# Performance work log

Measured on AMD Instinct MI355X. Metric: run time of the kernel, lower is better.

The kernel has to match this reference:

```python
import jax, jax.numpy as jnp
import numpy as np

NTOKENS = 50257
NHID = 1024
TPC = int(np.ceil(np.sqrt(NTOKENS)))          # 225 tokens per class
NCLASSES = int(np.ceil(NTOKENS / TPC))        # 224 classes
BATCH = 2048
INITRANGE = 0.1


def setup_inputs() -> dict:
    key = jax.random.key(0)
    k1, k2, k3, k4 = jax.random.split(key, 4)
    inputs = jax.random.normal(k1, (BATCH, NHID), dtype=jnp.float32)
    labels = jax.random.randint(k2, (BATCH,), 0, NTOKENS, dtype=jnp.int32)
    W_top = jax.random.uniform(k3, (NHID, NCLASSES), dtype=jnp.float32,
                               minval=-INITRANGE, maxval=INITRANGE)
    b_top = jnp.zeros((NCLASSES,), dtype=jnp.float32)
    W_bottom = jax.random.uniform(k4, (NCLASSES, NHID, TPC), dtype=jnp.float32,
                                  minval=-INITRANGE, maxval=INITRANGE)
    b_bottom = jnp.zeros((NCLASSES, TPC), dtype=jnp.float32)
    return {"inputs": inputs, "labels": labels, "W_top": W_top, "b_top": b_top,
            "W_bottom": W_bottom, "b_bottom": b_bottom}


def reference(inputs, labels, W_top, b_top, W_bottom, b_bottom):
    # Two-level hierarchical softmax: P(word) = P(class | h) * P(word | class, h)
    batch = inputs.shape[0]
    cls = labels // TPC          # [B] class index at top level
    word = labels % TPC          # [B] word index within class

    # Top level: [B, nclasses]
    top_probs = jax.nn.softmax(inputs @ W_top + b_top, axis=1)
    p_cls = top_probs[jnp.arange(batch), cls]            # [B]

    # Bottom level: gather per-example class weights then batched matvec
    Wb = W_bottom[cls]                                    # [B, nhid, tpc]
    bb = b_bottom[cls]                                    # [B, tpc]
    bottom_logits = jnp.einsum('bd,bdk->bk', inputs, Wb) + bb
    bottom_probs = jax.nn.softmax(bottom_logits, axis=1)
    p_word = bottom_probs[jnp.arange(batch), word]        # [B]

    return p_cls * p_word
```

## Files before the change

kernel.cpp:

```cpp
#include <hip/hip_runtime.h>
#include <math.h>

#define TPC 225
#define NCLS 224
#define NHID 1024
#define BATCH 2048
#define CAP 256

__global__ __launch_bounds__(256) void hs_bucket(const int* __restrict__ labels,
                                                 int* __restrict__ bucket,
                                                 int* __restrict__ cnt) {
    __shared__ int scnt[NCLS];
    const int t = threadIdx.x;
    for (int i = t; i < NCLS; i += 256) scnt[i] = 0;
    __syncthreads();
    for (int b = t; b < BATCH; b += 256) {
        int lab = labels[b];
        int c = lab / TPC;
        int w = lab - c * TPC;
        int pos = atomicAdd(&scnt[c], 1);
        bucket[c * CAP + pos] = (w << 16) | b;
    }
    __syncthreads();
    for (int i = t; i < NCLS; i += 256) cnt[i] = scnt[i];
}

template <int R, int WS, int NS>
__device__ __forceinline__ void gemm_softmax_rows(const float* const xrow[R],
                                                  const float* __restrict__ W,
                                                  const float* __restrict__ bias,
                                                  const int lane,
                                                  float prob[R][4]) {
    int kc[4];
#pragma unroll
    for (int j = 0; j < 4; j++) {
        int k = lane + 64 * j;
        kc[j] = (k < NS) ? k : (NS - 1);
    }
    float bs[4];
#pragma unroll
    for (int j = 0; j < 4; j++) bs[j] = bias[kc[j]];

    const float* wj[4];
#pragma unroll
    for (int j = 0; j < 4; j++) wj[j] = W + kc[j];
    const float* xr[R];
#pragma unroll
    for (int r = 0; r < R; r++) xr[r] = xrow[r];

    float wb[4][4][4];
    float4 xb[4][R];
    float acc[R][4];
#pragma unroll
    for (int r = 0; r < R; r++)
#pragma unroll
        for (int j = 0; j < 4; j++) acc[r][j] = 0.f;

#pragma unroll
    for (int b = 0; b < 4; b++) {
#pragma unroll
        for (int dd = 0; dd < 4; dd++)
#pragma unroll
            for (int j = 0; j < 4; j++) wb[b][dd][j] = wj[j][dd * WS];
#pragma unroll
        for (int r = 0; r < R; r++) xb[b][r] = *(const float4*)(xr[r]);
#pragma unroll
        for (int j = 0; j < 4; j++) wj[j] += 4 * WS;
#pragma unroll
        for (int r = 0; r < R; r++) xr[r] += 4;
    }

    for (int it = 0; it < 63; it++) {
#pragma unroll
        for (int b = 0; b < 4; b++) {
#pragma unroll
            for (int dd = 0; dd < 4; dd++)
#pragma unroll
                for (int r = 0; r < R; r++) {
                    float xv = ((const float*)&xb[b][r])[dd];
#pragma unroll
                    for (int j = 0; j < 4; j++)
                        acc[r][j] = fmaf(xv, wb[b][dd][j], acc[r][j]);
                }
#pragma unroll
            for (int dd = 0; dd < 4; dd++)
#pragma unroll
                for (int j = 0; j < 4; j++) wb[b][dd][j] = wj[j][dd * WS];
#pragma unroll
            for (int r = 0; r < R; r++) xb[b][r] = *(const float4*)(xr[r]);
#pragma unroll
            for (int j = 0; j < 4; j++) wj[j] += 4 * WS;
#pragma unroll
            for (int r = 0; r < R; r++) xr[r] += 4;
        }
    }

#pragma unroll
    for (int b = 0; b < 4; b++) {
#pragma unroll
        for (int dd = 0; dd < 4; dd++)
#pragma unroll
            for (int r = 0; r < R; r++) {
                float xv = ((const float*)&xb[b][r])[dd];
#pragma unroll
                for (int j = 0; j < 4; j++)
                    acc[r][j] = fmaf(xv, wb[b][dd][j], acc[r][j]);
            }
    }

#pragma unroll
    for (int r = 0; r < R; r++) {
        float lg[4];
#pragma unroll
        for (int j = 0; j < 4; j++) {
            int k = lane + 64 * j;
            lg[j] = (k < NS) ? acc[r][j] + bs[j] : -INFINITY;
        }
        float m = fmaxf(fmaxf(lg[0], lg[1]), fmaxf(lg[2], lg[3]));
#pragma unroll
        for (int off = 32; off > 0; off >>= 1) m = fmaxf(m, __shfl_xor(m, off, 64));
        float s = 0.f;
        float e[4];
#pragma unroll
        for (int j = 0; j < 4; j++) {
            int k = lane + 64 * j;
            e[j] = (k < NS) ? __expf(lg[j] - m) : 0.f;
            s += e[j];
        }
#pragma unroll
        for (int off = 32; off > 0; off >>= 1) s += __shfl_xor(s, off, 64);
        float inv = 1.f / s;
#pragma unroll
        for (int j = 0; j < 4; j++) prob[r][j] = e[j] * inv;
    }
}

__global__ __launch_bounds__(256, 1) void hs_top(const float* __restrict__ x,
                                                 const int* __restrict__ labels,
                                                 const float* __restrict__ W,
                                                 const float* __restrict__ bias,
                                                 float* __restrict__ pcls) {
    const int t = threadIdx.x;
    const int lane = t & 63;
    const int wave = t >> 6;
    const int r0 = blockIdx.x * 8 + wave * 2;

    const float* xrow[2] = {x + (size_t)r0 * NHID, x + (size_t)(r0 + 1) * NHID};
    float prob[2][4];
    gemm_softmax_rows<2, NCLS, NCLS>(xrow, W, bias, lane, prob);

#pragma unroll
    for (int r = 0; r < 2; r++) {
        int row = r0 + r;
        int c = labels[row] / TPC;
#pragma unroll
        for (int j = 0; j < 4; j++)
            if (lane + 64 * j == c) pcls[row] = prob[r][j];
    }
}

template <int R>
__device__ __forceinline__ void bottom_tile(const float* __restrict__ x,
                                            const float* __restrict__ Wc,
                                            const float* __restrict__ bbc,
                                            const int* __restrict__ bucket_c,
                                            const int n, const int base,
                                            const int lane, const int wave,
                                            const float* __restrict__ pcls,
                                            float* __restrict__ out) {
    const int i0 = base + wave * R;
    const float* xrow[R];
    int rowid[R], word[R];
#pragma unroll
    for (int r = 0; r < R; r++) {
        int idx = i0 + r;
        int packed = (idx < n) ? bucket_c[idx] : 0;
        rowid[r] = packed & 0xffff;
        word[r] = packed >> 16;
        xrow[r] = x + (size_t)rowid[r] * NHID;
    }
    float prob[R][4];
    gemm_softmax_rows<R, TPC, TPC>(xrow, Wc, bbc, lane, prob);
#pragma unroll
    for (int r = 0; r < R; r++) {
        if (i0 + r < n) {
#pragma unroll
            for (int j = 0; j < 4; j++)
                if (lane + 64 * j == word[r])
                    out[rowid[r]] = pcls[rowid[r]] * prob[r][j];
        }
    }
}

__global__ __launch_bounds__(256, 1) void hs_bottom(const float* __restrict__ x,
                                                    const float* __restrict__ Wb,
                                                    const float* __restrict__ bb,
                                                    const int* __restrict__ bucket,
                                                    const int* __restrict__ cnt,
                                                    const float* __restrict__ pcls,
                                                    float* __restrict__ out) {
    const int c = blockIdx.x;
    const int n = cnt[c];
    if (n == 0) return;
    const int t = threadIdx.x;
    const int lane = t & 63;
    const int wave = t >> 6;
    const float* Wc = Wb + (size_t)c * (NHID * TPC);
    const float* bbc = bb + c * TPC;
    const int* bucket_c = bucket + c * CAP;

    int R = (n + 3) >> 2;
    if (R > 8) R = 8;
    const int chunk = 4 * R;
    for (int base = 0; base < n; base += chunk) {
        switch (R) {
            case 1: bottom_tile<1>(x, Wc, bbc, bucket_c, n, base, lane, wave, pcls, out); break;
            case 2: bottom_tile<2>(x, Wc, bbc, bucket_c, n, base, lane, wave, pcls, out); break;
            case 3: bottom_tile<3>(x, Wc, bbc, bucket_c, n, base, lane, wave, pcls, out); break;
            case 4: bottom_tile<4>(x, Wc, bbc, bucket_c, n, base, lane, wave, pcls, out); break;
            case 5: bottom_tile<5>(x, Wc, bbc, bucket_c, n, base, lane, wave, pcls, out); break;
            case 6: bottom_tile<6>(x, Wc, bbc, bucket_c, n, base, lane, wave, pcls, out); break;
            case 7: bottom_tile<7>(x, Wc, bbc, bucket_c, n, base, lane, wave, pcls, out); break;
            default: bottom_tile<8>(x, Wc, bbc, bucket_c, n, base, lane, wave, pcls, out); break;
        }
    }
}

extern "C" void kernel_launch(void* const* d_in, const int* in_sizes, int n_in,
                              void* d_out, int out_size, void* d_ws, size_t ws_size,
                              hipStream_t stream) {
    const float* inputs   = (const float*)d_in[0];
    const int*   labels   = (const int*)d_in[1];
    const float* W_top    = (const float*)d_in[2];
    const float* b_top    = (const float*)d_in[3];
    const float* W_bottom = (const float*)d_in[4];
    const float* b_bottom = (const float*)d_in[5];
    float* out = (float*)d_out;

    int* bucket = (int*)d_ws;
    int* cnt    = bucket + NCLS * CAP;
    float* pcls = (float*)(cnt + NCLS);

    hs_bucket<<<1, 256, 0, stream>>>(labels, bucket, cnt);
    hs_top<<<BATCH / 8, 256, 0, stream>>>(inputs, labels, W_top, b_top, pcls);
    hs_bottom<<<NCLS, 256, 0, stream>>>(inputs, W_bottom, b_bottom, bucket, cnt,
                                        pcls, out);
}
```

Measured before the change: 467.4 us.

## Split logits GEMMs across column tiles and defer softmax to a finish kernel

Top and bottom logit computation now split output columns into four tiles per block, so each lane computes one column over several rows and the grid grows fourfold (NCLS*4 bottom blocks instead of NCLS). Raw logits go to a workspace buffer, and a new finish kernel applies bias, both softmaxes and the final product. Bottom-level rows are spread across waves in strips of up to four, with launch bounds raised to allow two blocks per CU. This aims to fix the poor parallelism of one block per class. The cost is an extra kernel launch, a workspace round trip of the logits, and re-reading x once per column tile.

Result: slower. 509.5 us (+9.0%).

```diff
diff --git a/kernel.cpp b/kernel.cpp
--- a/kernel.cpp
+++ b/kernel.cpp
@@ -6,6 +6,7 @@
 #define NHID 1024
 #define BATCH 2048
 #define CAP 256
+#define LSTRIDE 256
 
 __global__ __launch_bounds__(256) void hs_bucket(const int* __restrict__ labels,
                                                  int* __restrict__ bucket,
@@ -17,213 +18,202 @@
     for (int b = t; b < BATCH; b += 256) {
         int lab = labels[b];
         int c = lab / TPC;
-        int w = lab - c * TPC;
         int pos = atomicAdd(&scnt[c], 1);
-        bucket[c * CAP + pos] = (w << 16) | b;
+        bucket[c * CAP + pos] = b;
     }
     __syncthreads();
     for (int i = t; i < NCLS; i += 256) cnt[i] = scnt[i];
 }
 
-template <int R, int WS, int NS>
-__device__ __forceinline__ void gemm_softmax_rows(const float* const xrow[R],
-                                                  const float* __restrict__ W,
-                                                  const float* __restrict__ bias,
-                                                  const int lane,
-                                                  float prob[R][4]) {
-    int kc[4];
-#pragma unroll
-    for (int j = 0; j < 4; j++) {
-        int k = lane + 64 * j;
-        kc[j] = (k < NS) ? k : (NS - 1);
-    }
-    float bs[4];
-#pragma unroll
-    for (int j = 0; j < 4; j++) bs[j] = bias[kc[j]];
-
-    const float* wj[4];
-#pragma unroll
-    for (int j = 0; j < 4; j++) wj[j] = W + kc[j];
-    const float* xr[R];
-#pragma unroll
-    for (int r = 0; r < R; r++) xr[r] = xrow[r];
-
-    float wb[4][4][4];
-    float4 xb[4][R];
-    float acc[R][4];
-#pragma unroll
-    for (int r = 0; r < R; r++)
-#pragma unroll
-        for (int j = 0; j < 4; j++) acc[r][j] = 0.f;
-
-#pragma unroll
-    for (int b = 0; b < 4; b++) {
-#pragma unroll
-        for (int dd = 0; dd < 4; dd++)
-#pragma unroll
-            for (int j = 0; j < 4; j++) wb[b][dd][j] = wj[j][dd * WS];
-#pragma unroll
-        for (int r = 0; r < R; r++) xb[b][r] = *(const float4*)(xr[r]);
-#pragma unroll
-        for (int j = 0; j < 4; j++) wj[j] += 4 * WS;
-#pragma unroll
-        for (int r = 0; r < R; r++) xr[r] += 4;
-    }
-
-    for (int it = 0; it < 63; it++) {
-#pragma unroll
-        for (int b = 0; b < 4; b++) {
-#pragma unroll
-            for (int dd = 0; dd < 4; dd++)
-#pragma unroll
-                for (int r = 0; r < R; r++) {
-                    float xv = ((const float*)&xb[b][r])[dd];
-#pragma unroll
-                    for (int j = 0; j < 4; j++)
-                        acc[r][j] = fmaf(xv, wb[b][dd][j], acc[r][j]);
-                }
-#pragma unroll
-            for (int dd = 0; dd < 4; dd++)
-#pragma unroll
-                for (int j = 0; j < 4; j++) wb[b][dd][j] = wj[j][dd * WS];
-#pragma unroll
-            for (int r = 0; r < R; r++) xb[b][r] = *(const float4*)(xr[r]);
-#pragma unroll
-            for (int j = 0; j < 4; j++) wj[j] += 4 * WS;
-#pragma unroll
-            for (int r = 0; r < R; r++) xr[r] += 4;
-        }
-    }
-
-#pragma unroll
-    for (int b = 0; b < 4; b++) {
-#pragma unroll
-        for (int dd = 0; dd < 4; dd++)
+template <int R, int WS>
+__device__ __forceinline__ void kloop(const float* __restrict__ wp,
+                                      const float* const xp[R],
+                                      float acc[R]) {
+    constexpr int NG = NHID / 8;
+    float wv[4][8];
+    float4 xv[2][R][2];
+#pragma unroll
+    for (int r = 0; r < R; r++) acc[r] = 0.f;
+
+#pragma unroll
+    for (int b = 0; b < 4; b++)
+#pragma unroll
+        for (int u = 0; u < 8; u++) wv[b][u] = wp[(size_t)(b * 8 + u) * WS];
+#pragma unroll
+    for (int b = 0; b < 2; b++)
+#pragma unroll
+        for (int r = 0; r < R; r++) {
+            xv[b][r][0] = *(const float4*)(xp[r] + b * 8);
+            xv[b][r][1] = *(const float4*)(xp[r] + b * 8 + 4);
+        }
+    const float* wiss = wp + (size_t)32 * WS;
+    const float* xiss[R];
+#pragma unroll
+    for (int r = 0; r < R; r++) xiss[r] = xp[r] + 16;
+
+#pragma unroll 4
+    for (int g = 0; g < NG - 4; ++g) {
+        const int b = g & 3, xb = g & 1;
+#pragma unroll
+        for (int u = 0; u < 8; u++) {
+            const float w_u = wv[b][u];
 #pragma unroll
             for (int r = 0; r < R; r++) {
-                float xv = ((const float*)&xb[b][r])[dd];
-#pragma unroll
-                for (int j = 0; j < 4; j++)
-                    acc[r][j] = fmaf(xv, wb[b][dd][j], acc[r][j]);
+                const float xval = ((const float*)&xv[xb][r][u >> 2])[u & 3];
+                acc[r] = fmaf(xval, w_u, acc[r]);
             }
-    }
-
-#pragma unroll
-    for (int r = 0; r < R; r++) {
-        float lg[4];
-#pragma unroll
-        for (int j = 0; j < 4; j++) {
-            int k = lane + 64 * j;
-            lg[j] = (k < NS) ? acc[r][j] + bs[j] : -INFINITY;
-        }
-        float m = fmaxf(fmaxf(lg[0], lg[1]), fmaxf(lg[2], lg[3]));
-#pragma unroll
-        for (int off = 32; off > 0; off >>= 1) m = fmaxf(m, __shfl_xor(m, off, 64));
-        float s = 0.f;
-        float e[4];
-#pragma unroll
-        for (int j = 0; j < 4; j++) {
-            int k = lane + 64 * j;
-            e[j] = (k < NS) ? __expf(lg[j] - m) : 0.f;
-            s += e[j];
-        }
-#pragma unroll
-        for (int off = 32; off > 0; off >>= 1) s += __shfl_xor(s, off, 64);
-        float inv = 1.f / s;
-#pragma unroll
-        for (int j = 0; j < 4; j++) prob[r][j] = e[j] * inv;
-    }
-}
-
-__global__ __launch_bounds__(256, 1) void hs_top(const float* __restrict__ x,
-                                                 const int* __restrict__ labels,
-                                                 const float* __restrict__ W,
-                                                 const float* __restrict__ bias,
-                                                 float* __restrict__ pcls) {
+        }
+#pragma unroll
+        for (int u = 0; u < 8; u++) wv[b][u] = wiss[(size_t)u * WS];
+        wiss += 8 * WS;
+#pragma unroll
+        for (int r = 0; r < R; r++) {
+            xv[xb][r][0] = *(const float4*)(xiss[r]);
+            xv[xb][r][1] = *(const float4*)(xiss[r] + 4);
+            xiss[r] += 8;
+        }
+    }
+#pragma unroll
+    for (int g = NG - 4; g < NG; ++g) {
+        const int b = g & 3, xb = g & 1;
+#pragma unroll
+        for (int u = 0; u < 8; u++) {
+            const float w_u = wv[b][u];
+#pragma unroll
+            for (int r = 0; r < R; r++) {
+                const float xval = ((const float*)&xv[xb][r][u >> 2])[u & 3];
+                acc[r] = fmaf(xval, w_u, acc[r]);
+            }
+        }
+        if (g + 2 < NG) {
+#pragma unroll
+            for (int r = 0; r < R; r++) {
+                xv[xb][r][0] = *(const float4*)(xiss[r]);
+                xv[xb][r][1] = *(const float4*)(xiss[r] + 4);
+                xiss[r] += 8;
+            }
+        }
+    }
+}
+
+__global__ __launch_bounds__(256, 2) void hs_tlogits(const float* __restrict__ x,
+                                                     const float* __restrict__ W,
+                                                     float* __restrict__ tws) {
     const int t = threadIdx.x;
     const int lane = t & 63;
     const int wave = t >> 6;
-    const int r0 = blockIdx.x * 8 + wave * 2;
-
-    const float* xrow[2] = {x + (size_t)r0 * NHID, x + (size_t)(r0 + 1) * NHID};
-    float prob[2][4];
-    gemm_softmax_rows<2, NCLS, NCLS>(xrow, W, bias, lane, prob);
-
-#pragma unroll
-    for (int r = 0; r < 2; r++) {
-        int row = r0 + r;
-        int c = labels[row] / TPC;
-#pragma unroll
-        for (int j = 0; j < 4; j++)
-            if (lane + 64 * j == c) pcls[row] = prob[r][j];
+    const int r0 = (blockIdx.x >> 2) * 16 + wave * 4;
+    const int tile = blockIdx.x & 3;
+    const int col = tile * 56 + lane;
+    const int colc = (lane < 56) ? col : (NCLS - 1);
+
+    const float* xp[4];
+#pragma unroll
+    for (int r = 0; r < 4; r++) xp[r] = x + (size_t)(r0 + r) * NHID;
+    float acc[4];
+    kloop<4, NCLS>(W + colc, xp, acc);
+    if (lane < 56) {
+#pragma unroll
+        for (int r = 0; r < 4; r++) tws[(size_t)(r0 + r) * LSTRIDE + col] = acc[r];
     }
 }
 
 template <int R>
-__device__ __forceinline__ void bottom_tile(const float* __restrict__ x,
-                                            const float* __restrict__ Wc,
-                                            const float* __restrict__ bbc,
-                                            const int* __restrict__ bucket_c,
-                                            const int n, const int base,
-                                            const int lane, const int wave,
-                                            const float* __restrict__ pcls,
-                                            float* __restrict__ out) {
-    const int i0 = base + wave * R;
-    const float* xrow[R];
-    int rowid[R], word[R];
+__device__ __forceinline__ void btile(const float* __restrict__ x,
+                                      const float* __restrict__ Wcol,
+                                      const int* __restrict__ bucket_c,
+                                      const int base, const int col,
+                                      float* __restrict__ bws) {
+    int rowid[R];
+    const float* xp[R];
 #pragma unroll
     for (int r = 0; r < R; r++) {
-        int idx = i0 + r;
-        int packed = (idx < n) ? bucket_c[idx] : 0;
-        rowid[r] = packed & 0xffff;
-        word[r] = packed >> 16;
-        xrow[r] = x + (size_t)rowid[r] * NHID;
-    }
-    float prob[R][4];
-    gemm_softmax_rows<R, TPC, TPC>(xrow, Wc, bbc, lane, prob);
-#pragma unroll
-    for (int r = 0; r < R; r++) {
-        if (i0 + r < n) {
-#pragma unroll
-            for (int j = 0; j < 4; j++)
-                if (lane + 64 * j == word[r])
-                    out[rowid[r]] = pcls[rowid[r]] * prob[r][j];
-        }
-    }
-}
-
-__global__ __launch_bounds__(256, 1) void hs_bottom(const float* __restrict__ x,
-                                                    const float* __restrict__ Wb,
-                                                    const float* __restrict__ bb,
-                                                    const int* __restrict__ bucket,
-                                                    const int* __restrict__ cnt,
-                                                    const float* __restrict__ pcls,
-                                                    float* __restrict__ out) {
-    const int c = blockIdx.x;
-    const int n = cnt[c];
+        rowid[r] = __builtin_amdgcn_readfirstlane(bucket_c[base + r]);
+        xp[r] = x + (size_t)rowid[r] * NHID;
+    }
+    float acc[R];
+    kloop<R, TPC>(Wcol, xp, acc);
+    if (col < TPC) {
+#pragma unroll
+        for (int r = 0; r < R; r++) bws[(size_t)rowid[r] * LSTRIDE + col] = acc[r];
+    }
+}
+
+__global__ __launch_bounds__(256, 2) void hs_blogits(const float* __restrict__ x,
+                                                     const float* __restrict__ Wb,
+                                                     const int* __restrict__ bucket,
+                                                     const int* __restrict__ cnt,
+                                                     float* __restrict__ bws) {
+    const int c = blockIdx.x >> 2;
+    const int tile = blockIdx.x & 3;
+    const int n = __builtin_amdgcn_readfirstlane(cnt[c]);
     if (n == 0) return;
     const int t = threadIdx.x;
     const int lane = t & 63;
     const int wave = t >> 6;
-    const float* Wc = Wb + (size_t)c * (NHID * TPC);
-    const float* bbc = bb + c * TPC;
+    const int col = tile * 64 + lane;
+    const int colc = (col < TPC) ? col : (TPC - 1);
+    const float* Wcol = Wb + (size_t)c * (NHID * TPC) + colc;
     const int* bucket_c = bucket + c * CAP;
 
-    int R = (n + 3) >> 2;
-    if (R > 8) R = 8;
-    const int chunk = 4 * R;
-    for (int base = 0; base < n; base += chunk) {
+    const int nstrips = (n + 3) >> 2;
+    for (int s = wave; s < nstrips; s += 4) {
+        const int base = s * 4;
+        const int R = n - base < 4 ? n - base : 4;
         switch (R) {
-            case 1: bottom_tile<1>(x, Wc, bbc, bucket_c, n, base, lane, wave, pcls, out); break;
-            case 2: bottom_tile<2>(x, Wc, bbc, bucket_c, n, base, lane, wave, pcls, out); break;
-            case 3: bottom_tile<3>(x, Wc, bbc, bucket_c, n, base, lane, wave, pcls, out); break;
-            case 4: bottom_tile<4>(x, Wc, bbc, bucket_c, n, base, lane, wave, pcls, out); break;
-            case 5: bottom_tile<5>(x, Wc, bbc, bucket_c, n, base, lane, wave, pcls, out); break;
-            case 6: bottom_tile<6>(x, Wc, bbc, bucket_c, n, base, lane, wave, pcls, out); break;
-            case 7: bottom_tile<7>(x, Wc, bbc, bucket_c, n, base, lane, wave, pcls, out); break;
-            default: bottom_tile<8>(x, Wc, bbc, bucket_c, n, base, lane, wave, pcls, out); break;
-        }
-    }
+            case 1: btile<1>(x, Wcol, bucket_c, base, col, bws); break;
+            case 2: btile<2>(x, Wcol, bucket_c, base, col, bws); break;
+            case 3: btile<3>(x, Wcol, bucket_c, base, col, bws); break;
+            default: btile<4>(x, Wcol, bucket_c, base, col, bws); break;
+        }
+    }
+}
+
+__global__ __launch_bounds__(256) void hs_finish(const float* __restrict__ tws,
+                                                 const float* __restrict__ bws,
+                                                 const int* __restrict__ labels,
+                                                 const float* __restrict__ b_top,
+                                                 const float* __restrict__ b_bot,
+                                                 float* __restrict__ out) {
+    const int lane = threadIdx.x & 63;
+    const int wave = threadIdx.x >> 6;
+    const int row = blockIdx.x * 4 + wave;
+    const int label = labels[row];
+    const int c = label / TPC;
+    const int word = label - c * TPC;
+
+    float p[2];
+#pragma unroll
+    for (int lvl = 0; lvl < 2; lvl++) {
+        const int NS = lvl ? TPC : NCLS;
+        const int pick = lvl ? word : c;
+        const float* lws = lvl ? bws : tws;
+        const float* bias = lvl ? (b_bot + c * TPC) : b_top;
+        float lg[4];
+#pragma unroll
+        for (int j = 0; j < 4; j++) {
+            int k = lane + 64 * j;
+            lg[j] = (k < NS) ? lws[(size_t)row * LSTRIDE + k] + bias[k] : -INFINITY;
+        }
+        float m = fmaxf(fmaxf(lg[0], lg[1]), fmaxf(lg[2], lg[3]));
+#pragma unroll
+        for (int off = 32; off > 0; off >>= 1) m = fmaxf(m, __shfl_xor(m, off, 64));
+        float s = 0.f, pp = 0.f;
+#pragma unroll
+        for (int j = 0; j < 4; j++) {
+            int k = lane + 64 * j;
+            float e = (k < NS) ? __expf(lg[j] - m) : 0.f;
+            s += e;
+            if (k == pick) pp = e;
+        }
+#pragma unroll
+        for (int off = 32; off > 0; off >>= 1) {
+            s += __shfl_xor(s, off, 64);
+            pp += __shfl_xor(pp, off, 64);
+        }
+        p[lvl] = pp / s;
+    }
+    if (lane == 0) out[row] = p[0] * p[1];
 }
 
 extern "C" void kernel_launch(void* const* d_in, const int* in_sizes, int n_in,
@@ -239,10 +229,11 @@
 
     int* bucket = (int*)d_ws;
     int* cnt    = bucket + NCLS * CAP;
-    float* pcls = (float*)(cnt + NCLS);
+    float* tws  = (float*)(cnt + NCLS);
+    float* bws  = tws + (size_t)BATCH * LSTRIDE;
 
     hs_bucket<<<1, 256, 0, stream>>>(labels, bucket, cnt);
-    hs_top<<<BATCH / 8, 256, 0, stream>>>(inputs, labels, W_top, b_top, pcls);
-    hs_bottom<<<NCLS, 256, 0, stream>>>(inputs, W_bottom, b_bottom, bucket, cnt,
-                                        pcls, out);
-}
+    hs_tlogits<<<(BATCH / 16) * 4, 256, 0, stream>>>(inputs, W_top, tws);
+    hs_blogits<<<NCLS * 4, 256, 0, stream>>>(inputs, W_bottom, bucket, cnt, bws);
+    hs_finish<<<BATCH / 4, 256, 0, stream>>>(tws, bws, labels, b_top, b_bottom, out);
+}
```
